# Kernel optimization log

Hardware: AMD Instinct MI355X
Metric: run time of the kernel (lower is better)

Reference implementation:

```python
import jax, jax.numpy as jnp
import numpy as np

NUM_NODES = 100000
NUM_EDGES = 1600000
NUM_GRAPHS = 1000
NUM_FEATURES = 128
DIM = 32
NUM_CLASSES = 10


def setup_inputs() -> dict:
    key = jax.random.key(0)
    ks = jax.random.split(key, 20)
    inp = {
        "x": jax.random.normal(ks[0], (NUM_NODES, NUM_FEATURES), dtype=jnp.float32),
        "edge_index": jax.random.randint(ks[1], (2, NUM_EDGES), 0, NUM_NODES, dtype=jnp.int64),
        "batch": jnp.sort(jax.random.randint(ks[2], (NUM_NODES,), 0, NUM_GRAPHS, dtype=jnp.int64)),
        "edge_weight": jax.random.uniform(ks[3], (NUM_EDGES,), dtype=jnp.float32),
    }
    # GraphConv params: lin_rel (with bias) on aggregated msgs, lin_root (no bias) on x
    dims = [(NUM_FEATURES, DIM)] + [(DIM, DIM)] * 4
    for i, (fi, fo) in enumerate(dims, start=1):
        s = 1.0 / np.sqrt(fi)
        inp[f"Wrel{i}"] = jax.random.uniform(ks[3 + i], (fi, fo), jnp.float32, -s, s)
        inp[f"brel{i}"] = jax.random.uniform(ks[8 + i], (fo,), jnp.float32, -s, s)
        inp[f"Wroot{i}"] = jax.random.uniform(ks[13 + i], (fi, fo), jnp.float32, -s, s)
    s = 1.0 / np.sqrt(DIM)
    inp["Wlin1"] = jax.random.uniform(ks[19], (DIM, DIM), jnp.float32, -s, s)
    inp["blin1"] = jax.random.uniform(jax.random.fold_in(key, 100), (DIM,), jnp.float32, -s, s)
    inp["Wlin2"] = jax.random.uniform(jax.random.fold_in(key, 101), (DIM, NUM_CLASSES), jnp.float32, -s, s)
    inp["blin2"] = jax.random.uniform(jax.random.fold_in(key, 102), (NUM_CLASSES,), jnp.float32, -s, s)
    return inp


def _graph_conv(x, src, dst, ew, Wrel, brel, Wroot, num_nodes):
    # message: x_j * e_ji ; aggregate (add) at target ; out = lin_rel(agg) + lin_root(x)
    msg = x[src] * ew[:, None]                                   # [E, F_in]
    agg = jax.ops.segment_sum(msg, dst, num_segments=num_nodes)  # [N, F_in]
    return agg @ Wrel + brel + x @ Wroot


def reference(x, edge_index, batch, edge_weight,
              Wrel1, brel1, Wroot1, Wrel2, brel2, Wroot2,
              Wrel3, brel3, Wroot3, Wrel4, brel4, Wroot4,
              Wrel5, brel5, Wroot5, Wlin1, blin1, Wlin2, blin2):
    n = x.shape[0]
    src, dst = edge_index[0], edge_index[1]
    h = jax.nn.relu(_graph_conv(x, src, dst, edge_weight, Wrel1, brel1, Wroot1, n))
    h = jax.nn.relu(_graph_conv(h, src, dst, edge_weight, Wrel2, brel2, Wroot2, n))
    h = jax.nn.relu(_graph_conv(h, src, dst, edge_weight, Wrel3, brel3, Wroot3, n))
    h = jax.nn.relu(_graph_conv(h, src, dst, edge_weight, Wrel4, brel4, Wroot4, n))
    h = jax.nn.relu(_graph_conv(h, src, dst, edge_weight, Wrel5, brel5, Wroot5, n))
    g = jax.ops.segment_sum(h, batch, num_segments=NUM_GRAPHS)   # global_add_pool [G, DIM]
    g = jax.nn.relu(g @ Wlin1 + blin1)
    # dropout p=0.5 is identity in eval mode
    logits = g @ Wlin2 + blin2
    return jax.nn.log_softmax(logits, axis=-1)
```

## Files before the change

kernel.cpp:

```cpp
#include <hip/hip_runtime.h>
#include <stdint.h>

#define NN 100000
#define NE 1600000
#define NG 1000
#define FIN 128
#define DIM 32
#define NC 10

#define NBKT 512
#define NPB 196
#define BCAP 4608
#define RND 4096
#define CURS 16
#define NBINB 391
#define MM1P1 781
#define MM1P2 782

typedef unsigned int u32;
typedef __attribute__((ext_vector_type(8))) short short8;
typedef __attribute__((ext_vector_type(4))) float floatx4;
typedef __attribute__((ext_vector_type(4))) unsigned int uint4e;

__device__ __forceinline__ ushort f2bf(float f) {
    u32 b = __float_as_uint(f);
    return (ushort)((b + 0x7FFFu + ((b >> 16) & 1u)) >> 16);
}
__device__ __forceinline__ float bf2f(ushort u) {
    return __uint_as_float(((u32)u) << 16);
}

struct SBin {
    int cnt[NBKT]; int gbase[NBKT];
};
struct SCsr {
    int hist[NPB]; int base[NPB]; int wsum[4];
};
struct SMm {
    ushort xs[64 * 136];
};
union SMem1 { SBin b; SMm m; };
union SMem2 { SCsr c; SMm m; };

__global__ __launch_bounds__(256) void k_init(u32* __restrict__ zp, int zn,
        const float* __restrict__ W0r, const float* __restrict__ W0o,
        const float* __restrict__ W1r, const float* __restrict__ W1o,
        const float* __restrict__ W2r, const float* __restrict__ W2o,
        const float* __restrict__ W3r, const float* __restrict__ W3o,
        const float* __restrict__ W4r, const float* __restrict__ W4o,
        ushort* __restrict__ wfrag, ushort* __restrict__ wfrag1) {
    int i = blockIdx.x * 256 + threadIdx.x;
    if (i < zn) zp[i] = 0u;
    int t = threadIdx.x;
    int mat  = t >> 7;
    int nh   = (t >> 6) & 1;
    int lane = t & 63;
    int m = lane & 15;
    int g = lane >> 4;
    if (blockIdx.x < 4) {
        const float* Ws[8] = {W1r, W1o, W2r, W2o, W3r, W3o, W4r, W4o};
        const float* W = Ws[blockIdx.x * 2 + mat];
        ushort* dst = wfrag + (((size_t)blockIdx.x * 4 + mat * 2 + nh) * 64 + lane) * 8;
        #pragma unroll
        for (int j = 0; j < 8; ++j)
            dst[j] = f2bf(W[(g * 8 + j) * DIM + nh * 16 + m]);
    } else if (blockIdx.x < 8) {
        int kc = blockIdx.x - 4;
        const float* W = mat ? W0o : W0r;
        int nt = mat * 2 + nh;
        ushort* dst = wfrag1 + (((size_t)nt * 4 + kc) * 64 + lane) * 8;
        #pragma unroll
        for (int j = 0; j < 8; ++j)
            dst[j] = f2bf(W[(kc * 32 + g * 8 + j) * DIM + nh * 16 + m]);
    }
}

__device__ void bin_body(SMem1& sm, int blk, const int* __restrict__ ei,
        const float* __restrict__ ew, int* __restrict__ cursor,
        uint2* __restrict__ ebuf) {
    int tid = threadIdx.x;
    int e0 = blk * RND;
    int n  = min(RND, NE - e0);

    for (int i = tid; i < NBKT; i += 256) sm.b.cnt[i] = 0;
    __syncthreads();

    u32 pk[16], wvv[16], bp[16];
    #pragma unroll
    for (int q = 0; q < 16; ++q) {
        int i = tid + q * 256;
        bp[q] = 0xFFFFFFFFu;
        if (i < n) {
            int s = ei[e0 + i];
            int d = ei[NE + e0 + i];
            float w = ew[e0 + i];
            int b = d / NPB;
            int loc = d - b * NPB;
            int p = atomicAdd(&sm.b.cnt[b], 1);
            pk[q]  = (u32)s | ((u32)loc << 17);
            wvv[q] = __float_as_uint(w);
            bp[q]  = (u32)p | ((u32)b << 16);
        }
    }
    __syncthreads();

    for (int i = tid; i < NBKT; i += 256) {
        int c = sm.b.cnt[i];
        sm.b.gbase[i] = (c > 0) ? atomicAdd(&cursor[i * CURS], c) : 0;
    }
    __syncthreads();

    #pragma unroll
    for (int q = 0; q < 16; ++q) {
        if (bp[q] != 0xFFFFFFFFu) {
            int b = (int)(bp[q] >> 16);
            int p = (int)(bp[q] & 0xFFFFu);
            int pos = sm.b.gbase[b] + p;
            if (pos < BCAP) ebuf[(size_t)b * BCAP + pos] = make_uint2(pk[q], wvv[q]);
        }
    }
}

__device__ void csr_body(SMem2& sm, int bkt, const uint2* __restrict__ ebuf,
        u32* __restrict__ gbuf, const int* __restrict__ cursor, uint2* __restrict__ od) {
    int tid = threadIdx.x;
    int lane = tid & 63, wvx = tid >> 6;
    int cnt = min(cursor[bkt * CURS], 4096);
    for (int i = tid; i < NPB; i += 256) sm.c.hist[i] = 0;
    __syncthreads();
    const uint2* gb = ebuf + (size_t)bkt * BCAP;
    u32* gB = gbuf + (size_t)bkt * BCAP;
    uint2 my[16]; int mp[16];
    #pragma unroll
    for (int q = 0; q < 16; ++q) {
        int i = tid + q * 256;
        mp[q] = -1;
        if (i < cnt) {
            my[q] = gb[i];
            int loc = (int)(my[q].x >> 17);
            mp[q] = atomicAdd(&sm.c.hist[loc], 1);
        }
    }
    __syncthreads();
    int h  = (tid < NPB) ? sm.c.hist[tid] : 0;
    int hp = (h + 7) & ~7;
    int inc = hp;
    #pragma unroll
    for (int d = 1; d < 64; d <<= 1) {
        int u = __shfl_up(inc, d);
        if (lane >= d) inc += u;
    }
    if (lane == 63) sm.c.wsum[wvx] = inc;
    __syncthreads();
    int off = 0;
    #pragma unroll
    for (int w2 = 0; w2 < 3; ++w2) off += (w2 < wvx) ? sm.c.wsum[w2] : 0;
    if (tid < NPB) sm.c.base[tid] = off + inc - hp;
    __syncthreads();
    int tot = sm.c.wsum[0] + sm.c.wsum[1] + sm.c.wsum[2] + sm.c.wsum[3];
    tot = min(tot, BCAP);
    for (int i = tid; i < tot; i += 256) gB[i] = 0u;
    __syncthreads();
    #pragma unroll
    for (int q = 0; q < 16; ++q) {
        if (mp[q] >= 0) {
            int loc = (int)(my[q].x >> 17);
            int pos = sm.c.base[loc] + mp[q];
            if (pos < BCAP)
                gB[pos] = (my[q].x & 0x1FFFFu)
                        | ((u32)f2bf(__uint_as_float(my[q].y)) << 17);
        }
    }
    for (int i = tid; i < NPB; i += 256) {
        int node = bkt * NPB + i;
        if (node < NN) {
            int dg = sm.c.hist[i];
            int bs = sm.c.base[i];
            if (bs + ((dg + 7) & ~7) > BCAP) dg = max(0, BCAP - bs) & ~7;
            od[node] = make_uint2((u32)(bkt * BCAP + bs), (u32)dg);
        }
    }
}

__device__ void mm1_body(ushort* __restrict__ xs, int blk, const float* __restrict__ x,
        const ushort* __restrict__ wfrag1, const float* __restrict__ brel,
        ushort* __restrict__ ybf, ushort* __restrict__ aggb) {
    int tid = threadIdx.x;
    int base = blk * 64;
    for (int i = tid; i < 64 * 32; i += 256) {
        int r = i >> 5, c = i & 31;
        int node = base + r;
        float4 v = make_float4(0.f, 0.f, 0.f, 0.f);
        if (node < NN) v = ((const float4*)x)[(size_t)node * 32 + c];
        ushort4 u;
        u.x = f2bf(v.x); u.y = f2bf(v.y); u.z = f2bf(v.z); u.w = f2bf(v.w);
        *(ushort4*)&xs[r * 136 + c * 4] = u;
    }
    int lane = tid & 63;
    int w = tid >> 6;
    int m = lane & 15;
    int q = lane >> 4;
    short8 bfr[4][4];
    #pragma unroll
    for (int nt = 0; nt < 4; ++nt)
        #pragma unroll
        for (int kc = 0; kc < 4; ++kc)
            bfr[nt][kc] = *(const short8*)&wfrag1[(((size_t)nt * 4 + kc) * 64 + lane) * 8];
    __syncthreads();
    floatx4 acc[4] = {{0.f,0.f,0.f,0.f},{0.f,0.f,0.f,0.f},{0.f,0.f,0.f,0.f},{0.f,0.f,0.f,0.f}};
    #pragma unroll
    for (int kc = 0; kc < 4; ++kc) {
        short8 af = *(const short8*)&xs[(w * 16 + m) * 136 + kc * 32 + q * 8];
        #pragma unroll
        for (int nt = 0; nt < 4; ++nt)
            acc[nt] = __builtin_amdgcn_mfma_f32_16x16x32_bf16(af, bfr[nt][kc], acc[nt], 0, 0, 0);
    }
    float br0 = brel[m], br1 = brel[16 + m];
    #pragma unroll
    for (int reg = 0; reg < 4; ++reg) {
        int row = q * 4 + reg;
        int node = base + w * 16 + row;
        if (node < NN) {
            ybf[(size_t)node * 32 + m]       = f2bf(acc[0][reg]);
            ybf[(size_t)node * 32 + 16 + m]  = f2bf(acc[1][reg]);
            aggb[(size_t)node * 32 + m]      = f2bf(acc[2][reg] + br0);
            aggb[(size_t)node * 32 + 16 + m] = f2bf(acc[3][reg] + br1);
        }
    }
}

__global__ __launch_bounds__(256, 8) void k_pre1(const int* __restrict__ ei,
        const float* __restrict__ ew, int* __restrict__ cursor, uint2* __restrict__ ebuf,
        const float* __restrict__ x, const ushort* __restrict__ wfrag1,
        const float* __restrict__ brel,
        ushort* __restrict__ ybf, ushort* __restrict__ aggb) {
    __shared__ SMem1 sm;
    if (blockIdx.x < NBINB) bin_body(sm, blockIdx.x, ei, ew, cursor, ebuf);
    else                    mm1_body(sm.m.xs, blockIdx.x - NBINB, x, wfrag1, brel, ybf, aggb);
}

__global__ __launch_bounds__(256, 8) void k_pre2(const uint2* __restrict__ ebuf,
        u32* __restrict__ gbuf, const int* __restrict__ cursor, uint2* __restrict__ od,
        const float* __restrict__ x, const ushort* __restrict__ wfrag1,
        const float* __restrict__ brel,
        ushort* __restrict__ ybf, ushort* __restrict__ aggb) {
    __shared__ SMem2 sm;
    if (blockIdx.x < NBKT) csr_body(sm, blockIdx.x, ebuf, gbuf, cursor, od);
    else                   mm1_body(sm.m.xs, blockIdx.x - NBKT + MM1P1, x, wfrag1, brel, ybf, aggb);
}

__device__ __forceinline__ float2 gather_accum(const u32* __restrict__ eb, int deg,
        const uint* __restrict__ ybp) {
    float acc0 = 0.f, acc1 = 0.f;
    int b = 0;
    for (; b + 8 < deg; b += 16) {
        const uint4e* p = (const uint4e*)(eb + b);
        uint4e a0 = __builtin_nontemporal_load(p + 0);
        uint4e a1 = __builtin_nontemporal_load(p + 1);
        uint4e a2 = __builtin_nontemporal_load(p + 2);
        uint4e a3 = __builtin_nontemporal_load(p + 3);
        uint u0  = ybp[(a0.x & 0x1FFFFu) << 4];
        uint u1  = ybp[(a0.y & 0x1FFFFu) << 4];
        uint u2  = ybp[(a0.z & 0x1FFFFu) << 4];
        uint u3  = ybp[(a0.w & 0x1FFFFu) << 4];
        uint u4  = ybp[(a1.x & 0x1FFFFu) << 4];
        uint u5  = ybp[(a1.y & 0x1FFFFu) << 4];
        uint u6  = ybp[(a1.z & 0x1FFFFu) << 4];
        uint u7  = ybp[(a1.w & 0x1FFFFu) << 4];
        uint u8  = ybp[(a2.x & 0x1FFFFu) << 4];
        uint u9  = ybp[(a2.y & 0x1FFFFu) << 4];
        uint u10 = ybp[(a2.z & 0x1FFFFu) << 4];
        uint u11 = ybp[(a2.w & 0x1FFFFu) << 4];
        uint u12 = ybp[(a3.x & 0x1FFFFu) << 4];
        uint u13 = ybp[(a3.y & 0x1FFFFu) << 4];
        uint u14 = ybp[(a3.z & 0x1FFFFu) << 4];
        uint u15 = ybp[(a3.w & 0x1FFFFu) << 4];
        float w;
        w = __uint_as_float((a0.x & 0xFFFE0000u) >> 1);
        acc0 += w * __uint_as_float(u0 << 16);  acc1 += w * __uint_as_float(u0 & 0xFFFF0000u);
        w = __uint_as_float((a0.y & 0xFFFE0000u) >> 1);
        acc0 += w * __uint_as_float(u1 << 16);  acc1 += w * __uint_as_float(u1 & 0xFFFF0000u);
        w = __uint_as_float((a0.z & 0xFFFE0000u) >> 1);
        acc0 += w * __uint_as_float(u2 << 16);  acc1 += w * __uint_as_float(u2 & 0xFFFF0000u);
        w = __uint_as_float((a0.w & 0xFFFE0000u) >> 1);
        acc0 += w * __uint_as_float(u3 << 16);  acc1 += w * __uint_as_float(u3 & 0xFFFF0000u);
        w = __uint_as_float((a1.x & 0xFFFE0000u) >> 1);
        acc0 += w * __uint_as_float(u4 << 16);  acc1 += w * __uint_as_float(u4 & 0xFFFF0000u);
        w = __uint_as_float((a1.y & 0xFFFE0000u) >> 1);
        acc0 += w * __uint_as_float(u5 << 16);  acc1 += w * __uint_as_float(u5 & 0xFFFF0000u);
        w = __uint_as_float((a1.z & 0xFFFE0000u) >> 1);
        acc0 += w * __uint_as_float(u6 << 16);  acc1 += w * __uint_as_float(u6 & 0xFFFF0000u);
        w = __uint_as_float((a1.w & 0xFFFE0000u) >> 1);
        acc0 += w * __uint_as_float(u7 << 16);  acc1 += w * __uint_as_float(u7 & 0xFFFF0000u);
        w = __uint_as_float((a2.x & 0xFFFE0000u) >> 1);
        acc0 += w * __uint_as_float(u8 << 16);  acc1 += w * __uint_as_float(u8 & 0xFFFF0000u);
        w = __uint_as_float((a2.y & 0xFFFE0000u) >> 1);
        acc0 += w * __uint_as_float(u9 << 16);  acc1 += w * __uint_as_float(u9 & 0xFFFF0000u);
        w = __uint_as_float((a2.z & 0xFFFE0000u) >> 1);
        acc0 += w * __uint_as_float(u10 << 16); acc1 += w * __uint_as_float(u10 & 0xFFFF0000u);
        w = __uint_as_float((a2.w & 0xFFFE0000u) >> 1);
        acc0 += w * __uint_as_float(u11 << 16); acc1 += w * __uint_as_float(u11 & 0xFFFF0000u);
        w = __uint_as_float((a3.x & 0xFFFE0000u) >> 1);
        acc0 += w * __uint_as_float(u12 << 16); acc1 += w * __uint_as_float(u12 & 0xFFFF0000u);
        w = __uint_as_float((a3.y & 0xFFFE0000u) >> 1);
        acc0 += w * __uint_as_float(u13 << 16); acc1 += w * __uint_as_float(u13 & 0xFFFF0000u);
        w = __uint_as_float((a3.z & 0xFFFE0000u) >> 1);
        acc0 += w * __uint_as_float(u14 << 16); acc1 += w * __uint_as_float(u14 & 0xFFFF0000u);
        w = __uint_as_float((a3.w & 0xFFFE0000u) >> 1);
        acc0 += w * __uint_as_float(u15 << 16); acc1 += w * __uint_as_float(u15 & 0xFFFF0000u);
    }
    if (b < deg) {
        const uint4e* p = (const uint4e*)(eb + b);
        uint4e a0 = __builtin_nontemporal_load(p + 0);
        uint4e a1 = __builtin_nontemporal_load(p + 1);
        uint u0 = ybp[(a0.x & 0x1FFFFu) << 4];
        uint u1 = ybp[(a0.y & 0x1FFFFu) << 4];
        uint u2 = ybp[(a0.z & 0x1FFFFu) << 4];
        uint u3 = ybp[(a0.w & 0x1FFFFu) << 4];
        uint u4 = ybp[(a1.x & 0x1FFFFu) << 4];
        uint u5 = ybp[(a1.y & 0x1FFFFu) << 4];
        uint u6 = ybp[(a1.z & 0x1FFFFu) << 4];
        uint u7 = ybp[(a1.w & 0x1FFFFu) << 4];
        float w;
        w = __uint_as_float((a0.x & 0xFFFE0000u) >> 1);
        acc0 += w * __uint_as_float(u0 << 16);  acc1 += w * __uint_as_float(u0 & 0xFFFF0000u);
        w = __uint_as_float((a0.y & 0xFFFE0000u) >> 1);
        acc0 += w * __uint_as_float(u1 << 16);  acc1 += w * __uint_as_float(u1 & 0xFFFF0000u);
        w = __uint_as_float((a0.z & 0xFFFE0000u) >> 1);
        acc0 += w * __uint_as_float(u2 << 16);  acc1 += w * __uint_as_float(u2 & 0xFFFF0000u);
        w = __uint_as_float((a0.w & 0xFFFE0000u) >> 1);
        acc0 += w * __uint_as_float(u3 << 16);  acc1 += w * __uint_as_float(u3 & 0xFFFF0000u);
        w = __uint_as_float((a1.x & 0xFFFE0000u) >> 1);
        acc0 += w * __uint_as_float(u4 << 16);  acc1 += w * __uint_as_float(u4 & 0xFFFF0000u);
        w = __uint_as_float((a1.y & 0xFFFE0000u) >> 1);
        acc0 += w * __uint_as_float(u5 << 16);  acc1 += w * __uint_as_float(u5 & 0xFFFF0000u);
        w = __uint_as_float((a1.z & 0xFFFE0000u) >> 1);
        acc0 += w * __uint_as_float(u6 << 16);  acc1 += w * __uint_as_float(u6 & 0xFFFF0000u);
        w = __uint_as_float((a1.w & 0xFFFE0000u) >> 1);
        acc0 += w * __uint_as_float(u7 << 16);  acc1 += w * __uint_as_float(u7 & 0xFFFF0000u);
    }
    return make_float2(acc0, acc1);
}

__global__ __launch_bounds__(256, 6) void k_gfused(const ushort* __restrict__ ybf,
        const u32* __restrict__ gbuf, const uint2* __restrict__ od,
        const ushort* __restrict__ aggb, const ushort* __restrict__ wfragL,
        const float* __restrict__ brel,
        ushort* __restrict__ ybf_n, ushort* __restrict__ aggb_n) {
    __shared__ __align__(16) ushort hsm[16 * 40];
    int tid  = threadIdx.x;
    int w    = tid >> 6;
    int lane = tid & 63;
    int nl   = lane >> 4;
    int fp   = lane & 15;
    int node = blockIdx.x * 16 + w * 4 + nl;
    short8 bfr = *(const short8*)&wfragL[((size_t)w * 64 + lane) * 8];
    uint2 o = od[node];
    const u32* eb = gbuf + o.x;
    const uint* ybp = (const uint*)ybf + fp;
    uint pa = ((const uint*)aggb)[node * 16 + fp];
    float2 ac = gather_accum(eb, (int)o.y, ybp);
    float h0 = fmaxf(__uint_as_float(pa << 16) + ac.x, 0.f);
    float h1 = fmaxf(__uint_as_float(pa & 0xFFFF0000u) + ac.y, 0.f);
    u32 hp = (u32)f2bf(h0) | ((u32)f2bf(h1) << 16);
    *(u32*)&hsm[(w * 4 + nl) * 40 + fp * 2] = hp;
    __syncthreads();
    short8 af = *(const short8*)&hsm[(lane & 15) * 40 + (lane >> 4) * 8];
    floatx4 acc = {0.f, 0.f, 0.f, 0.f};
    acc = __builtin_amdgcn_mfma_f32_16x16x32_bf16(af, bfr, acc, 0, 0, 0);
    int ncol  = (w & 1) * 16 + (lane & 15);
    int drow0 = (lane >> 4) * 4;
    size_t obase = ((size_t)blockIdx.x * 16 + drow0) * DIM + ncol;
    if (w < 2) {
        #pragma unroll
        for (int r = 0; r < 4; ++r)
            ybf_n[obase + (size_t)r * DIM] = f2bf(acc[r]);
    } else {
        float bb = brel[ncol];
        #pragma unroll
        for (int r = 0; r < 4; ++r)
            aggb_n[obase + (size_t)r * DIM] = f2bf(acc[r] + bb);
    }
}

__global__ __launch_bounds__(256, 6) void k_glast_pool(const ushort* __restrict__ ybf,
        const u32* __restrict__ gbuf, const uint2* __restrict__ od,
        const ushort* __restrict__ aggb, const int* __restrict__ batch,
        float* __restrict__ g) {
    __shared__ __align__(16) float hsm[16][34];
    int tid  = threadIdx.x;
    int w    = tid >> 6;
    int lane = tid & 63;
    int nl   = lane >> 4;
    int fp   = lane & 15;
    int node = blockIdx.x * 16 + w * 4 + nl;
    uint2 o = od[node];
    const u32* eb = gbuf + o.x;
    const uint* ybp = (const uint*)ybf + fp;
    uint pa = ((const uint*)aggb)[node * 16 + fp];
    float2 ac = gather_accum(eb, (int)o.y, ybp);
    float2 hv;
    hv.x = fmaxf(__uint_as_float(pa << 16) + ac.x, 0.f);
    hv.y = fmaxf(__uint_as_float(pa & 0xFFFF0000u) + ac.y, 0.f);
    *(float2*)&hsm[w * 4 + nl][fp * 2] = hv;
    __syncthreads();
    if (tid < 32) {
        int nb = blockIdx.x * 16;
        int curb = batch[nb];
        float run = 0.f;
        #pragma unroll
        for (int n = 0; n < 16; ++n) {
            int b = batch[nb + n];
            if (b != curb) {
                atomicAdd(&g[(size_t)curb * DIM + tid], run);
                run = 0.f; curb = b;
            }
            run += hsm[n][tid];
        }
        atomicAdd(&g[(size_t)curb * DIM + tid], run);
    }
}

__global__ __launch_bounds__(64) void k_head(const float* __restrict__ g,
        const float* __restrict__ W1, const float* __restrict__ b1,
        const float* __restrict__ W2, const float* __restrict__ b2,
        float* __restrict__ out) {
    __shared__ float gs[DIM];
    __shared__ float a1[DIM];
    __shared__ float lg[NC];
    int t = threadIdx.x;
    int gr = blockIdx.x;
    if (t < DIM) gs[t] = g[(size_t)gr * DIM + t];
    __syncthreads();
    if (t < DIM) {
        float a = b1[t];
        #pragma unroll
        for (int k = 0; k < DIM; ++k) a += gs[k] * W1[k * DIM + t];
        a1[t] = fmaxf(a, 0.f);
    }
    __syncthreads();
    if (t < NC) {
        float a = b2[t];
        #pragma unroll
        for (int k = 0; k < DIM; ++k) a += a1[k] * W2[k * NC + t];
        lg[t] = a;
    }
    __syncthreads();
    if (t == 0) {
        float m = lg[0];
        for (int c = 1; c < NC; ++c) m = fmaxf(m, lg[c]);
        float s = 0.f;
        for (int c = 0; c < NC; ++c) s += expf(lg[c] - m);
        float ls = m + logf(s);
        for (int c = 0; c < NC; ++c) out[(size_t)gr * NC + c] = lg[c] - ls;
    }
}

extern "C" void kernel_launch(void* const* d_in, const int* in_sizes, int n_in,
                              void* d_out, int out_size, void* d_ws, size_t ws_size,
                              hipStream_t stream) {
    const float* x     = (const float*)d_in[0];
    const int*   ei    = (const int*)d_in[1];
    const int*   batch = (const int*)d_in[2];
    const float* ew    = (const float*)d_in[3];
    const float* Wrel[5]  = {(const float*)d_in[4],  (const float*)d_in[7],  (const float*)d_in[10], (const float*)d_in[13], (const float*)d_in[16]};
    const float* brel[5]  = {(const float*)d_in[5],  (const float*)d_in[8],  (const float*)d_in[11], (const float*)d_in[14], (const float*)d_in[17]};
    const float* Wroot[5] = {(const float*)d_in[6],  (const float*)d_in[9],  (const float*)d_in[12], (const float*)d_in[15], (const float*)d_in[18]};
    const float* W1 = (const float*)d_in[19];
    const float* b1 = (const float*)d_in[20];
    const float* W2 = (const float*)d_in[21];
    const float* b2 = (const float*)d_in[22];
    float* out = (float*)d_out;

    char* ws = (char*)d_ws;
    const size_t off_cursor = 0;
    const size_t off_g      = 32768;
    const size_t zero_end   = 160768;
    const size_t off_wfrag  = 160768;
    const size_t off_wfrag1 = 177152;
    const size_t off_ebuf   = 193536;
    const size_t ebuf_bytes = ((size_t)NBKT * BCAP + 64) * 8;
    const size_t off_gbuf   = off_ebuf + ebuf_bytes;
    const size_t gbuf_bytes = ((size_t)NBKT * BCAP + 64) * 4;
    const size_t off_od     = off_gbuf + gbuf_bytes;
    const size_t off_A      = off_od + (size_t)NN * 8;
    const size_t off_C      = off_A + (size_t)NN * DIM * 2;
    const size_t off_B1     = off_C + (size_t)NN * DIM * 2;
    const size_t off_B2     = off_B1 + (size_t)NN * DIM * 2;
    const size_t need       = off_B2 + (size_t)NN * DIM * 2;
    if (ws_size < need) return;

    int*    cursor = (int*)(ws + off_cursor);
    float*  g      = (float*)(ws + off_g);
    ushort* wfrag  = (ushort*)(ws + off_wfrag);
    ushort* wfrag1 = (ushort*)(ws + off_wfrag1);
    uint2*  ebuf   = (uint2*)(ws + off_ebuf);
    u32*    gbuf   = (u32*)(ws + off_gbuf);
    uint2*  od     = (uint2*)(ws + off_od);
    ushort* A      = (ushort*)(ws + off_A);
    ushort* C      = (ushort*)(ws + off_C);
    ushort* B1     = (ushort*)(ws + off_B1);
    ushort* B2     = (ushort*)(ws + off_B2);

    int zcount = (int)(zero_end / 4);
    k_init<<<(zcount + 255) / 256, 256, 0, stream>>>((u32*)ws, zcount,
        Wrel[0], Wroot[0], Wrel[1], Wroot[1], Wrel[2], Wroot[2],
        Wrel[3], Wroot[3], Wrel[4], Wroot[4], wfrag, wfrag1);

    k_pre1<<<NBINB + MM1P1, 256, 0, stream>>>(ei, ew, cursor, ebuf,
                                              x, wfrag1, brel[0], B1, A);
    k_pre2<<<NBKT + MM1P2, 256, 0, stream>>>(ebuf, gbuf, cursor, od,
                                             x, wfrag1, brel[0], B1, A);

    const int ngt = NN / 16;
    ushort* aggc = A;  ushort* aggn = C;
    ushort* yc   = B1; ushort* yn   = B2;
    for (int L = 1; L < 5; ++L) {
        k_gfused<<<ngt, 256, 0, stream>>>(yc, gbuf, od, aggc,
                                          wfrag + (size_t)(L - 1) * 2048, brel[L], yn, aggn);
        ushort* tf = aggc; aggc = aggn; aggn = tf;
        ushort* tu = yc; yc = yn; yn = tu;
    }
    k_glast_pool<<<ngt, 256, 0, stream>>>(yc, gbuf, od, aggc, batch, g);
    k_head<<<NG, 64, 0, stream>>>(g, W1, b1, W2, b2, out);
}
```

Baseline: 307.2 us.

## Replace bucketed two-pass CSR build with global degree count, scan, atomic scatter

The shared-memory bucket binning and per-bucket CSR construction are replaced by a global CSR build: a per-node degree histogram using global atomics, a three-kernel prefix scan of padded degrees, and an atomic-cursor scatter of packed (src, bf16 weight) edges straight into the final gather buffer. This removes the intermediate 8-byte edge buffer and its extra read/write pass, and drops the bucket capacity limits that could truncate edges. In exchange it adds three small launches, 1.6M global atomics on random addresses, and a memset of the whole gather buffer in the init kernel. Edge order within each node now depends on atomic scheduling. The gather kernels' launch bounds are also raised from 6 to 8 blocks per SM.

```diff
diff --git a/kernel.cpp b/kernel.cpp
--- a/kernel.cpp
+++ b/kernel.cpp
@@ -8,14 +8,12 @@
 #define DIM 32
 #define NC 10
 
-#define NBKT 512
-#define NPB 196
-#define BCAP 4608
 #define RND 4096
-#define CURS 16
-#define NBINB 391
+#define NSCB 391
 #define MM1P1 781
 #define MM1P2 782
+#define NDEG 100352
+#define GCAP 2300064
 
 typedef unsigned int u32;
 typedef __attribute__((ext_vector_type(8))) short short8;
@@ -30,19 +28,8 @@
     return __uint_as_float(((u32)u) << 16);
 }
 
-struct SBin {
-    int cnt[NBKT]; int gbase[NBKT];
-};
-struct SCsr {
-    int hist[NPB]; int base[NPB]; int wsum[4];
-};
-struct SMm {
-    ushort xs[64 * 136];
-};
-union SMem1 { SBin b; SMm m; };
-union SMem2 { SCsr c; SMm m; };
-
-__global__ __launch_bounds__(256) void k_init(u32* __restrict__ zp, int zn,
+__global__ __launch_bounds__(256) void k_init(u32* __restrict__ zp1, int zn1,
+        u32* __restrict__ zp2, int zn2,
         const float* __restrict__ W0r, const float* __restrict__ W0o,
         const float* __restrict__ W1r, const float* __restrict__ W1o,
         const float* __restrict__ W2r, const float* __restrict__ W2o,
@@ -50,7 +37,8 @@
         const float* __restrict__ W4r, const float* __restrict__ W4o,
         ushort* __restrict__ wfrag, ushort* __restrict__ wfrag1) {
     int i = blockIdx.x * 256 + threadIdx.x;
-    if (i < zn) zp[i] = 0u;
+    if (i < zn1) zp1[i] = 0u;
+    if (i < zn2) zp2[i] = 0u;
     int t = threadIdx.x;
     int mat  = t >> 7;
     int nh   = (t >> 6) & 1;
@@ -72,113 +60,6 @@
         #pragma unroll
         for (int j = 0; j < 8; ++j)
             dst[j] = f2bf(W[(kc * 32 + g * 8 + j) * DIM + nh * 16 + m]);
-    }
-}
-
-__device__ void bin_body(SMem1& sm, int blk, const int* __restrict__ ei,
-        const float* __restrict__ ew, int* __restrict__ cursor,
-        uint2* __restrict__ ebuf) {
-    int tid = threadIdx.x;
-    int e0 = blk * RND;
-    int n  = min(RND, NE - e0);
-
-    for (int i = tid; i < NBKT; i += 256) sm.b.cnt[i] = 0;
-    __syncthreads();
-
-    u32 pk[16], wvv[16], bp[16];
-    #pragma unroll
-    for (int q = 0; q < 16; ++q) {
-        int i = tid + q * 256;
-        bp[q] = 0xFFFFFFFFu;
-        if (i < n) {
-            int s = ei[e0 + i];
-            int d = ei[NE + e0 + i];
-            float w = ew[e0 + i];
-            int b = d / NPB;
-            int loc = d - b * NPB;
-            int p = atomicAdd(&sm.b.cnt[b], 1);
-            pk[q]  = (u32)s | ((u32)loc << 17);
-            wvv[q] = __float_as_uint(w);
-            bp[q]  = (u32)p | ((u32)b << 16);
-        }
-    }
-    __syncthreads();
-
-    for (int i = tid; i < NBKT; i += 256) {
-        int c = sm.b.cnt[i];
-        sm.b.gbase[i] = (c > 0) ? atomicAdd(&cursor[i * CURS], c) : 0;
-    }
-    __syncthreads();
-
-    #pragma unroll
-    for (int q = 0; q < 16; ++q) {
-        if (bp[q] != 0xFFFFFFFFu) {
-            int b = (int)(bp[q] >> 16);
-            int p = (int)(bp[q] & 0xFFFFu);
-            int pos = sm.b.gbase[b] + p;
-            if (pos < BCAP) ebuf[(size_t)b * BCAP + pos] = make_uint2(pk[q], wvv[q]);
-        }
-    }
-}
-
-__device__ void csr_body(SMem2& sm, int bkt, const uint2* __restrict__ ebuf,
-        u32* __restrict__ gbuf, const int* __restrict__ cursor, uint2* __restrict__ od) {
-    int tid = threadIdx.x;
-    int lane = tid & 63, wvx = tid >> 6;
-    int cnt = min(cursor[bkt * CURS], 4096);
-    for (int i = tid; i < NPB; i += 256) sm.c.hist[i] = 0;
-    __syncthreads();
-    const uint2* gb = ebuf + (size_t)bkt * BCAP;
-    u32* gB = gbuf + (size_t)bkt * BCAP;
-    uint2 my[16]; int mp[16];
-    #pragma unroll
-    for (int q = 0; q < 16; ++q) {
-        int i = tid + q * 256;
-        mp[q] = -1;
-        if (i < cnt) {
-            my[q] = gb[i];
-            int loc = (int)(my[q].x >> 17);
-            mp[q] = atomicAdd(&sm.c.hist[loc], 1);
-        }
-    }
-    __syncthreads();
-    int h  = (tid < NPB) ? sm.c.hist[tid] : 0;
-    int hp = (h + 7) & ~7;
-    int inc = hp;
-    #pragma unroll
-    for (int d = 1; d < 64; d <<= 1) {
-        int u = __shfl_up(inc, d);
-        if (lane >= d) inc += u;
-    }
-    if (lane == 63) sm.c.wsum[wvx] = inc;
-    __syncthreads();
-    int off = 0;
-    #pragma unroll
-    for (int w2 = 0; w2 < 3; ++w2) off += (w2 < wvx) ? sm.c.wsum[w2] : 0;
-    if (tid < NPB) sm.c.base[tid] = off + inc - hp;
-    __syncthreads();
-    int tot = sm.c.wsum[0] + sm.c.wsum[1] + sm.c.wsum[2] + sm.c.wsum[3];
-    tot = min(tot, BCAP);
-    for (int i = tid; i < tot; i += 256) gB[i] = 0u;
-    __syncthreads();
-    #pragma unroll
-    for (int q = 0; q < 16; ++q) {
-        if (mp[q] >= 0) {
-            int loc = (int)(my[q].x >> 17);
-            int pos = sm.c.base[loc] + mp[q];
-            if (pos < BCAP)
-                gB[pos] = (my[q].x & 0x1FFFFu)
-                        | ((u32)f2bf(__uint_as_float(my[q].y)) << 17);
-        }
-    }
-    for (int i = tid; i < NPB; i += 256) {
-        int node = bkt * NPB + i;
-        if (node < NN) {
-            int dg = sm.c.hist[i];
-            int bs = sm.c.base[i];
-            if (bs + ((dg + 7) & ~7) > BCAP) dg = max(0, BCAP - bs) & ~7;
-            od[node] = make_uint2((u32)(bkt * BCAP + bs), (u32)dg);
-        }
     }
 }
 
@@ -229,24 +110,116 @@
     }
 }
 
-__global__ __launch_bounds__(256, 8) void k_pre1(const int* __restrict__ ei,
-        const float* __restrict__ ew, int* __restrict__ cursor, uint2* __restrict__ ebuf,
+__global__ __launch_bounds__(256, 8) void k_cnt(const int* __restrict__ ei,
+        int* __restrict__ deg,
         const float* __restrict__ x, const ushort* __restrict__ wfrag1,
         const float* __restrict__ brel,
         ushort* __restrict__ ybf, ushort* __restrict__ aggb) {
-    __shared__ SMem1 sm;
-    if (blockIdx.x < NBINB) bin_body(sm, blockIdx.x, ei, ew, cursor, ebuf);
-    else                    mm1_body(sm.m.xs, blockIdx.x - NBINB, x, wfrag1, brel, ybf, aggb);
-}
-
-__global__ __launch_bounds__(256, 8) void k_pre2(const uint2* __restrict__ ebuf,
-        u32* __restrict__ gbuf, const int* __restrict__ cursor, uint2* __restrict__ od,
+    __shared__ ushort xs[64 * 136];
+    if (blockIdx.x < NSCB) {
+        int tid = threadIdx.x;
+        int e0 = blockIdx.x * RND;
+        int n  = min(RND, NE - e0);
+        #pragma unroll
+        for (int q = 0; q < 16; ++q) {
+            int i = tid + q * 256;
+            if (i < n) {
+                int d = ei[NE + e0 + i];
+                atomicAdd(&deg[d], 1);
+            }
+        }
+    } else {
+        mm1_body(xs, blockIdx.x - NSCB, x, wfrag1, brel, ybf, aggb);
+    }
+}
+
+__global__ __launch_bounds__(256) void k_scanA(const int* __restrict__ deg,
+        int* __restrict__ bsum) {
+    __shared__ int ws4[4];
+    int t = threadIdx.x, lane = t & 63, w = t >> 6;
+    int4 v = ((const int4*)deg)[blockIdx.x * 256 + t];
+    int s = ((v.x + 7) & ~7) + ((v.y + 7) & ~7) + ((v.z + 7) & ~7) + ((v.w + 7) & ~7);
+    int inc = s;
+    #pragma unroll
+    for (int d = 1; d < 64; d <<= 1) {
+        int u = __shfl_up(inc, d);
+        if (lane >= d) inc += u;
+    }
+    if (lane == 63) ws4[w] = inc;
+    __syncthreads();
+    if (t == 0) bsum[blockIdx.x] = ws4[0] + ws4[1] + ws4[2] + ws4[3];
+}
+
+__global__ __launch_bounds__(128) void k_scanB(const int* __restrict__ bsum,
+        int* __restrict__ boffs) {
+    __shared__ int ws2[2];
+    int t = threadIdx.x, lane = t & 63, w = t >> 6;
+    int v = (t < 98) ? bsum[t] : 0;
+    int inc = v;
+    #pragma unroll
+    for (int d = 1; d < 64; d <<= 1) {
+        int u = __shfl_up(inc, d);
+        if (lane >= d) inc += u;
+    }
+    if (lane == 63) ws2[w] = inc;
+    __syncthreads();
+    int off = (w == 1) ? ws2[0] : 0;
+    if (t < 98) boffs[t] = off + inc - v;
+}
+
+__global__ __launch_bounds__(256) void k_scanC(int* __restrict__ deg,
+        const int* __restrict__ boffs, uint2* __restrict__ od) {
+    __shared__ int ws4[4];
+    int t = threadIdx.x, lane = t & 63, w = t >> 6;
+    int nb = blockIdx.x * 1024 + t * 4;
+    int4 v = ((const int4*)deg)[blockIdx.x * 256 + t];
+    int p0 = (v.x + 7) & ~7, p1 = (v.y + 7) & ~7, p2 = (v.z + 7) & ~7, p3 = (v.w + 7) & ~7;
+    int s = p0 + p1 + p2 + p3;
+    int inc = s;
+    #pragma unroll
+    for (int d = 1; d < 64; d <<= 1) {
+        int u = __shfl_up(inc, d);
+        if (lane >= d) inc += u;
+    }
+    if (lane == 63) ws4[w] = inc;
+    __syncthreads();
+    int off = boffs[blockIdx.x];
+    #pragma unroll
+    for (int w2 = 0; w2 < 3; ++w2) off += (w2 < w) ? ws4[w2] : 0;
+    int ex = off + inc - s;
+    if (nb + 0 < NN) od[nb + 0] = make_uint2((u32)ex, (u32)v.x);
+    if (nb + 1 < NN) od[nb + 1] = make_uint2((u32)(ex + p0), (u32)v.y);
+    if (nb + 2 < NN) od[nb + 2] = make_uint2((u32)(ex + p0 + p1), (u32)v.z);
+    if (nb + 3 < NN) od[nb + 3] = make_uint2((u32)(ex + p0 + p1 + p2), (u32)v.w);
+    ((int4*)deg)[blockIdx.x * 256 + t] = make_int4(0, 0, 0, 0);
+}
+
+__global__ __launch_bounds__(256, 8) void k_scat(const int* __restrict__ ei,
+        const float* __restrict__ ew, int* __restrict__ deg,
+        const uint2* __restrict__ od, u32* __restrict__ gbuf,
         const float* __restrict__ x, const ushort* __restrict__ wfrag1,
         const float* __restrict__ brel,
         ushort* __restrict__ ybf, ushort* __restrict__ aggb) {
-    __shared__ SMem2 sm;
-    if (blockIdx.x < NBKT) csr_body(sm, blockIdx.x, ebuf, gbuf, cursor, od);
-    else                   mm1_body(sm.m.xs, blockIdx.x - NBKT + MM1P1, x, wfrag1, brel, ybf, aggb);
+    __shared__ ushort xs[64 * 136];
+    if (blockIdx.x < NSCB) {
+        int tid = threadIdx.x;
+        int e0 = blockIdx.x * RND;
+        int n  = min(RND, NE - e0);
+        #pragma unroll
+        for (int q = 0; q < 16; ++q) {
+            int i = tid + q * 256;
+            if (i < n) {
+                int s = ei[e0 + i];
+                int d = ei[NE + e0 + i];
+                float wv = ew[e0 + i];
+                int r = atomicAdd(&deg[d], 1);
+                u32 base = ((const u32*)od)[(size_t)d * 2];
+                gbuf[base + r] = (u32)s | ((u32)f2bf(wv) << 17);
+            }
+        }
+    } else {
+        mm1_body(xs, blockIdx.x - NSCB + MM1P1, x, wfrag1, brel, ybf, aggb);
+    }
 }
 
 __device__ __forceinline__ float2 gather_accum(const u32* __restrict__ eb, int deg,
@@ -342,7 +315,7 @@
     return make_float2(acc0, acc1);
 }
 
-__global__ __launch_bounds__(256, 6) void k_gfused(const ushort* __restrict__ ybf,
+__global__ __launch_bounds__(256, 8) void k_gfused(const ushort* __restrict__ ybf,
         const u32* __restrict__ gbuf, const uint2* __restrict__ od,
         const ushort* __restrict__ aggb, const ushort* __restrict__ wfragL,
         const float* __restrict__ brel,
@@ -383,7 +356,7 @@
     }
 }
 
-__global__ __launch_bounds__(256, 6) void k_glast_pool(const ushort* __restrict__ ybf,
+__global__ __launch_bounds__(256, 8) void k_glast_pool(const ushort* __restrict__ ybf,
         const u32* __restrict__ gbuf, const uint2* __restrict__ od,
         const ushort* __restrict__ aggb, const int* __restrict__ batch,
         float* __restrict__ g) {
@@ -473,43 +446,47 @@
     float* out = (float*)d_out;
 
     char* ws = (char*)d_ws;
-    const size_t off_cursor = 0;
-    const size_t off_g      = 32768;
-    const size_t zero_end   = 160768;
-    const size_t off_wfrag  = 160768;
-    const size_t off_wfrag1 = 177152;
-    const size_t off_ebuf   = 193536;
-    const size_t ebuf_bytes = ((size_t)NBKT * BCAP + 64) * 8;
-    const size_t off_gbuf   = off_ebuf + ebuf_bytes;
-    const size_t gbuf_bytes = ((size_t)NBKT * BCAP + 64) * 4;
-    const size_t off_od     = off_gbuf + gbuf_bytes;
-    const size_t off_A      = off_od + (size_t)NN * 8;
+    const size_t off_deg    = 0;
+    const size_t off_g      = 401408;
+    const size_t zlow_end   = 529408;
+    const size_t off_bsum   = 529408;
+    const size_t off_boffs  = 529920;
+    const size_t off_wfrag  = 530432;
+    const size_t off_wfrag1 = 546816;
+    const size_t off_od     = 563200;
+    const size_t off_gbuf   = 1363200;
+    const size_t off_A      = off_gbuf + (size_t)GCAP * 4;
     const size_t off_C      = off_A + (size_t)NN * DIM * 2;
     const size_t off_B1     = off_C + (size_t)NN * DIM * 2;
     const size_t off_B2     = off_B1 + (size_t)NN * DIM * 2;
     const size_t need       = off_B2 + (size_t)NN * DIM * 2;
     if (ws_size < need) return;
 
-    int*    cursor = (int*)(ws + off_cursor);
+    int*    deg    = (int*)(ws + off_deg);
     float*  g      = (float*)(ws + off_g);
+    int*    bsum   = (int*)(ws + off_bsum);
+    int*    boffs  = (int*)(ws + off_boffs);
     ushort* wfrag  = (ushort*)(ws + off_wfrag);
     ushort* wfrag1 = (ushort*)(ws + off_wfrag1);
-    uint2*  ebuf   = (uint2*)(ws + off_ebuf);
+    uint2*  od     = (uint2*)(ws + off_od);
     u32*    gbuf   = (u32*)(ws + off_gbuf);
-    uint2*  od     = (uint2*)(ws + off_od);
     ushort* A      = (ushort*)(ws + off_A);
     ushort* C      = (ushort*)(ws + off_C);
     ushort* B1     = (ushort*)(ws + off_B1);
     ushort* B2     = (ushort*)(ws + off_B2);
 
-    int zcount = (int)(zero_end / 4);
-    k_init<<<(zcount + 255) / 256, 256, 0, stream>>>((u32*)ws, zcount,
+    int zn1 = (int)(zlow_end / 4);
+    int zn2 = GCAP;
+    int zgrid = (GCAP + 255) / 256;
+    k_init<<<zgrid, 256, 0, stream>>>((u32*)ws, zn1, (u32*)gbuf, zn2,
         Wrel[0], Wroot[0], Wrel[1], Wroot[1], Wrel[2], Wroot[2],
         Wrel[3], Wroot[3], Wrel[4], Wroot[4], wfrag, wfrag1);
 
-    k_pre1<<<NBINB + MM1P1, 256, 0, stream>>>(ei, ew, cursor, ebuf,
-                                              x, wfrag1, brel[0], B1, A);
-    k_pre2<<<NBKT + MM1P2, 256, 0, stream>>>(ebuf, gbuf, cursor, od,
+    k_cnt<<<NSCB + MM1P1, 256, 0, stream>>>(ei, deg, x, wfrag1, brel[0], B1, A);
+    k_scanA<<<98, 256, 0, stream>>>(deg, bsum);
+    k_scanB<<<1, 128, 0, stream>>>(bsum, boffs);
+    k_scanC<<<98, 256, 0, stream>>>(deg, boffs, od);
+    k_scat<<<NSCB + MM1P2, 256, 0, stream>>>(ei, ew, deg, od, gbuf,
                                              x, wfrag1, brel[0], B1, A);
 
     const int ngt = NN / 16;
```

After: 440.1 us. +43.3%, slower.
